# Kernel optimization log

Measured on AMD Instinct MI355X. Metric: run time of the kernel, lower is better.

The kernel has to match this reference:

```python
import jax, jax.numpy as jnp
import numpy as np
from jax import lax

B, N_SITES, FEAT, BOND, OUT = 2048, 128, 64, 32, 256
CORE_SCALE = 0.02  # keeps the 128-step matrix product finite


def setup_inputs() -> dict:
    key = jax.random.key(0)
    ks = jax.random.split(key, 6)
    return {
        "x": jax.random.normal(ks[0], (B, N_SITES, FEAT), dtype=jnp.float32),
        "cores": jax.random.normal(ks[1], (N_SITES, BOND, FEAT, BOND), dtype=jnp.float32) * CORE_SCALE,
        "start": jax.random.normal(ks[2], (1, BOND), dtype=jnp.float32),
        "end": jax.random.normal(ks[3], (BOND, 1), dtype=jnp.float32),
        "fc_w": jax.random.normal(ks[4], (OUT, 1), dtype=jnp.float32),
        "fc_b": jax.random.normal(ks[5], (OUT,), dtype=jnp.float32),
    }


def reference(x, cores, start, end, fc_w, fc_b):
    # x: [B, N, F]; cores: [N, D, F, D]; start: [1, D]; end: [D, 1]
    b = x.shape[0]
    res0 = jnp.broadcast_to(start, (b, start.shape[1]))  # [B, D]

    def step(res, site):
        xi, core = site  # xi: [B, F], core: [D, F, D]
        m = jnp.einsum('bf,dfr->bdr', xi, core)  # per-site transfer matrix [B, D, D]
        return jnp.einsum('bd,bdr->br', res, m), None

    res, _ = lax.scan(step, res0, (jnp.swapaxes(x, 0, 1), cores))
    val = res @ end  # [B, 1]
    return val @ fc_w.T + fc_b  # [B, OUT]
```

## Files before the change

### kernel.cpp

```cpp
#include <hip/hip_runtime.h>


#define NSITES 128
#define FEATD  64
#define BOND   32
#define OUTD   256
#define BT     16
#define SEGLEN 16
#define NSEG   (NSITES / SEGLEN)
#define NBT    (2048 / BT)

#define RSTRIDE 48
#define BSTRIDE 1552

typedef __attribute__((ext_vector_type(4))) float float4v;

__device__ __forceinline__ unsigned pk4_fp8(float a, float b, float c, float d) {
    int v = __builtin_amdgcn_cvt_pk_fp8_f32(a, b, 0, false);
    v = __builtin_amdgcn_cvt_pk_fp8_f32(c, d, v, true);
    return (unsigned)v;
}

__global__ __launch_bounds__(256)
void prep_cores8(const float* __restrict__ cores, unsigned char* __restrict__ core8) {
    __shared__ float tile[FEATD][BOND + 4];
    const int nd = blockIdx.x;
    const int t  = threadIdx.x;
    const float* src = cores + (size_t)nd * (FEATD * BOND);
    {
        int base = t * 8;
        int f = base >> 5, r0 = base & 31;
        float4 v0 = *(const float4*)(src + base);
        float4 v1 = *(const float4*)(src + base + 4);
        tile[f][r0 + 0] = v0.x; tile[f][r0 + 1] = v0.y;
        tile[f][r0 + 2] = v0.z; tile[f][r0 + 3] = v0.w;
        tile[f][r0 + 4] = v1.x; tile[f][r0 + 5] = v1.y;
        tile[f][r0 + 6] = v1.z; tile[f][r0 + 7] = v1.w;
    }
    __syncthreads();
    const int r = t >> 3, f0 = (t & 7) * 8;
    const float s = 16.0f;
    unsigned lo = pk4_fp8(tile[f0 + 0][r] * s, tile[f0 + 1][r] * s,
                          tile[f0 + 2][r] * s, tile[f0 + 3][r] * s);
    unsigned hi = pk4_fp8(tile[f0 + 4][r] * s, tile[f0 + 5][r] * s,
                          tile[f0 + 6][r] * s, tile[f0 + 7][r] * s);
    uint2 w; w.x = lo; w.y = hi;
    *(uint2*)(core8 + ((size_t)nd * BOND + r) * FEATD + f0) = w;
}

__global__ __launch_bounds__(512, 4)
void mps_seg(const float* __restrict__ x, const unsigned char* __restrict__ core8,
             unsigned char* __restrict__ Pout) {
    __shared__ __align__(16) unsigned char MS[BT * BSTRIDE];
    __shared__ __align__(16) unsigned char PS[BT * BSTRIDE];
    __shared__ __align__(16) unsigned char XS[BT * 72];

    const int t    = threadIdx.x;
    const int wave = t >> 6;
    const int lane = t & 63;
    const int cl   = lane & 15;
    const int q    = lane >> 4;
    const int bt   = blockIdx.x;
    const int seg  = blockIdx.y;
    const int b0   = bt * BT;

    {
        int b = t >> 5, d = t & 31;
        unsigned w[8];
#pragma unroll
        for (int dw = 0; dw < 8; ++dw)
            w[dw] = ((d >> 2) == dw) ? (0x58u << ((d & 3) * 8)) : 0u;
        uint4* p = (uint4*)&PS[b * BSTRIDE + d * RSTRIDE];
        p[0] = make_uint4(w[0], w[1], w[2], w[3]);
        p[1] = make_uint4(w[4], w[5], w[6], w[7]);
    }

    const int xb = t >> 5, xf = (t & 31) * 2;
    float2 xf2 = *(const float2*)(x + ((size_t)(b0 + xb) * NSITES + seg * SEGLEN) * FEATD + xf);

    for (int k = 0; k < SEGLEN; ++k) {
        const int n = seg * SEGLEN + k;

        long af[16];
        {
            const unsigned char* base = core8 + (size_t)n * (1024 * FEATD);
#pragma unroll
            for (int i = 0; i < 8; ++i) {
                const unsigned char* p =
                    base + (size_t)((wave * 8 + i) * 16 + cl) * FEATD + q * 8;
                af[i * 2 + 0] = *(const long*)p;
                af[i * 2 + 1] = *(const long*)(p + 32);
            }
        }

        {
            int v = __builtin_amdgcn_cvt_pk_fp8_f32(xf2.x, xf2.y, 0, false);
            *(unsigned short*)&XS[xb * 72 + xf] = (unsigned short)(v & 0xffff);
        }
        __syncthreads();

        long bx0 = *(const long*)&XS[cl * 72 + q * 8];
        long bx1 = *(const long*)&XS[cl * 72 + 32 + q * 8];
        float4v acc[8];
#pragma unroll
        for (int i = 0; i < 8; ++i) {
            float4v z = {0.f, 0.f, 0.f, 0.f};
            z = __builtin_amdgcn_mfma_f32_16x16x32_fp8_fp8(af[i * 2 + 0], bx0, z, 0, 0, 0);
            acc[i] = __builtin_amdgcn_mfma_f32_16x16x32_fp8_fp8(af[i * 2 + 1], bx1, z, 0, 0, 0);
        }

#pragma unroll
        for (int p = 0; p < 2; ++p)
#pragma unroll
            for (int g = 0; g < 4; ++g) {
                unsigned w = pk4_fp8(acc[0 + p][g], acc[2 + p][g],
                                     acc[4 + p][g], acc[6 + p][g]);
                *(unsigned*)&MS[cl * BSTRIDE + (16 * p + 4 * q + g) * RSTRIDE + wave * 4] = w;
            }

        if (k + 1 < SEGLEN)
            xf2 = *(const float2*)(x + ((size_t)(b0 + xb) * NSITES + n + 1) * FEATD + xf);

        __syncthreads();

        long pa[2][2], pb[2][2];
#pragma unroll
        for (int bi = 0; bi < 2; ++bi) {
            int bb = wave * 2 + bi;
#pragma unroll
            for (int h = 0; h < 2; ++h) {
                pa[bi][h] = *(const long*)&MS[bb * BSTRIDE + (h * 16 + cl) * RSTRIDE + q * 8];
                pb[bi][h] = *(const long*)&PS[bb * BSTRIDE + (h * 16 + cl) * RSTRIDE + q * 8];
            }
        }
        float4v pacc[2][2][2];
#pragma unroll
        for (int bi = 0; bi < 2; ++bi)
#pragma unroll
            for (int I = 0; I < 2; ++I)
#pragma unroll
                for (int J = 0; J < 2; ++J) {
                    float4v z = {0.f, 0.f, 0.f, 0.f};
                    pacc[bi][I][J] =
                        __builtin_amdgcn_mfma_f32_16x16x32_fp8_fp8(pa[bi][I], pb[bi][J], z, 0, 0, 0);
                }
#pragma unroll
        for (int bi = 0; bi < 2; ++bi) {
            int bb = wave * 2 + bi;
#pragma unroll
            for (int I = 0; I < 2; ++I)
#pragma unroll
                for (int J = 0; J < 2; ++J) {
                    float4v c = pacc[bi][I][J];
                    unsigned w = pk4_fp8(c[0] * 0.0625f, c[1] * 0.0625f,
                                         c[2] * 0.0625f, c[3] * 0.0625f);
                    *(unsigned*)&PS[bb * BSTRIDE + (J * 16 + cl) * RSTRIDE + I * 16 + q * 4] = w;
                }
        }
    }

    __syncthreads();
    {
        int b = t >> 5, d = t & 31;
        const uint4* p = (const uint4*)&PS[b * BSTRIDE + d * RSTRIDE];
        uint4* g = (uint4*)(Pout + (((size_t)seg * 2048 + b0 + b) * 1024 + d * 32));
        g[0] = p[0];
        g[1] = p[1];
    }
}

__global__ __launch_bounds__(256)
void combine(const unsigned char* __restrict__ Pout, const float* __restrict__ startv,
             const float* __restrict__ endv, const float* __restrict__ fc_w,
             const float* __restrict__ fc_b, float* __restrict__ out) {
    __shared__ __align__(16) unsigned char st[8 * 1024];
    __shared__ float resA[8][33], resB[8][33];
    __shared__ float val[8];
    const int t  = threadIdx.x;
    const int b0 = blockIdx.x * 8;
    const int bb = t >> 5, r = t & 31;

    resA[bb][r] = startv[r];
    for (int s = 0; s < NSEG; ++s) {
        {
            const uint4* g = (const uint4*)(Pout + ((size_t)s * 2048 + b0) * 1024 + (size_t)t * 32);
            uint4* p = (uint4*)&st[t * 32];
            p[0] = g[0];
            p[1] = g[1];
        }
        __syncthreads();
        const float* rin = (s & 1) ? &resB[bb][0] : &resA[bb][0];
        float* rout      = (s & 1) ? &resA[bb][0] : &resB[bb][0];
        float acc = 0.f;
#pragma unroll
        for (int d = 0; d < BOND; ++d) {
            int byte = st[bb * 1024 + d * 32 + r];
            acc += rin[d] * __builtin_amdgcn_cvt_f32_fp8(byte, 0);
        }
        rout[r] = acc * 0.0625f;
        __syncthreads();
    }
    float prod = resA[bb][r] * endv[r];
#pragma unroll
    for (int off = 16; off >= 1; off >>= 1) prod += __shfl_down(prod, off, 32);
    if (r == 0) val[bb] = prod;
    __syncthreads();

    const float v = val[t >> 5];
    const int j0 = (t & 31) * 8;
    const int ob = b0 + (t >> 5);
#pragma unroll
    for (int i = 0; i < 2; ++i) {
        int j = j0 + i * 4;
        float4 w4 = *(const float4*)(fc_w + j);
        float4 bbv = *(const float4*)(fc_b + j);
        float4 o;
        o.x = v * w4.x + bbv.x;
        o.y = v * w4.y + bbv.y;
        o.z = v * w4.z + bbv.z;
        o.w = v * w4.w + bbv.w;
        *(float4*)(out + (size_t)ob * OUTD + j) = o;
    }
}

extern "C" void kernel_launch(void* const* d_in, const int* in_sizes, int n_in,
                              void* d_out, int out_size, void* d_ws, size_t ws_size,
                              hipStream_t stream) {
    const float* x      = (const float*)d_in[0];
    const float* cores  = (const float*)d_in[1];
    const float* startv = (const float*)d_in[2];
    const float* endv   = (const float*)d_in[3];
    const float* fc_w   = (const float*)d_in[4];
    const float* fc_b   = (const float*)d_in[5];
    float* out = (float*)d_out;

    unsigned char* core8 = (unsigned char*)d_ws;
    unsigned char* Pout  = core8 + (size_t)NSITES * 1024 * FEATD;

    prep_cores8<<<NSITES * BOND, 256, 0, stream>>>(cores, core8);
    mps_seg<<<dim3(NBT, NSEG), 512, 0, stream>>>(x, core8, Pout);
    combine<<<2048 / 8, 256, 0, stream>>>(Pout, startv, endv, fc_w, fc_b, out);
}
```

Measured before the change: 244.5 us.

## Process two sites per iteration and keep running product in registers

```diff
diff --git a/kernel.cpp b/kernel.cpp
--- a/kernel.cpp
+++ b/kernel.cpp
@@ -8,10 +8,11 @@
 #define BT     16
 #define SEGLEN 16
 #define NSEG   (NSITES / SEGLEN)
+#define NPAIR  (SEGLEN / 2)
 #define NBT    (2048 / BT)
 
-#define RSTRIDE 48
-#define BSTRIDE 1552
+#define RSTRIDE 36
+#define BSTRIDE 1164
 
 typedef __attribute__((ext_vector_type(4))) float float4v;
 
@@ -19,6 +20,37 @@
     int v = __builtin_amdgcn_cvt_pk_fp8_f32(a, b, 0, false);
     v = __builtin_amdgcn_cvt_pk_fp8_f32(c, d, v, true);
     return (unsigned)v;
+}
+
+__device__ __forceinline__ long ld8(const unsigned char* p) {
+    unsigned lo = *(const unsigned*)p;
+    unsigned hi = *(const unsigned*)(p + 4);
+    return (long)(((unsigned long long)hi << 32) | (unsigned long long)lo);
+}
+
+__device__ __forceinline__ void af_load(long af[16], const unsigned char* __restrict__ core8,
+                                        int n, int wave, int cl, int q) {
+    const unsigned char* base = core8 + (size_t)n * (1024 * FEATD);
+#pragma unroll
+    for (int i = 0; i < 8; ++i) {
+        const unsigned char* p = base + (size_t)((wave * 8 + i) * 16 + cl) * FEATD + q * 8;
+        af[2 * i + 0] = *(const long*)p;
+        af[2 * i + 1] = *(const long*)(p + 32);
+    }
+}
+
+__device__ __forceinline__ long cvt_frag(float4v c0, float4v c1,
+                                         int idxlo, int idxhi, int selhi) {
+    const float s = 0.0625f;
+    int d0 = (int)pk4_fp8(c0[0] * s, c0[1] * s, c0[2] * s, c0[3] * s);
+    int d1 = (int)pk4_fp8(c1[0] * s, c1[1] * s, c1[2] * s, c1[3] * s);
+    int l0 = __builtin_amdgcn_ds_bpermute(idxlo, d0);
+    int l1 = __builtin_amdgcn_ds_bpermute(idxlo, d1);
+    int h0 = __builtin_amdgcn_ds_bpermute(idxhi, d0);
+    int h1 = __builtin_amdgcn_ds_bpermute(idxhi, d1);
+    unsigned lo = (unsigned)(selhi ? l1 : l0);
+    unsigned hi = (unsigned)(selhi ? h1 : h0);
+    return (long)(((unsigned long long)hi << 32) | (unsigned long long)lo);
 }
 
 __global__ __launch_bounds__(256)
@@ -51,9 +83,10 @@
 __global__ __launch_bounds__(512, 4)
 void mps_seg(const float* __restrict__ x, const unsigned char* __restrict__ core8,
              unsigned char* __restrict__ Pout) {
-    __shared__ __align__(16) unsigned char MS[BT * BSTRIDE];
-    __shared__ __align__(16) unsigned char PS[BT * BSTRIDE];
-    __shared__ __align__(16) unsigned char XS[BT * 72];
+    __shared__ __align__(16) unsigned char MA[BT * BSTRIDE];
+    __shared__ __align__(16) unsigned char MB[BT * BSTRIDE];
+    __shared__ __align__(16) unsigned char NT[BT * BSTRIDE];
+    __shared__ __align__(16) unsigned char XS[2][2][BT * 72];
 
     const int t    = threadIdx.x;
     const int wave = t >> 6;
@@ -63,109 +96,152 @@
     const int bt   = blockIdx.x;
     const int seg  = blockIdx.y;
     const int b0   = bt * BT;
-
+    const int xb   = t >> 5, xf = (t & 31) * 2;
+
+    const int idxlo = (cl + 16 * ((2 * q) & 3)) << 2;
+    const int idxhi = (cl + 16 * ((2 * q + 1) & 3)) << 2;
+    const int selhi = q >> 1;
+
+    long ps[2][2];
+#pragma unroll
+    for (int J = 0; J < 2; ++J) {
+        int row = J * 16 + cl;
+        int jj  = row - 8 * q;
+        long v  = (jj >= 0 && jj < 8) ? (long)(0x58ULL << (8 * jj)) : 0L;
+        ps[0][J] = v;
+        ps[1][J] = v;
+    }
+
+    const int n0 = seg * SEGLEN;
+
+    const float* xptr = x + ((size_t)(b0 + xb) * NSITES + n0) * FEATD + xf;
+    float2 xa  = *(const float2*)xptr;
+    float2 xbv = *(const float2*)(xptr + FEATD);
     {
-        int b = t >> 5, d = t & 31;
-        unsigned w[8];
-#pragma unroll
-        for (int dw = 0; dw < 8; ++dw)
-            w[dw] = ((d >> 2) == dw) ? (0x58u << ((d & 3) * 8)) : 0u;
-        uint4* p = (uint4*)&PS[b * BSTRIDE + d * RSTRIDE];
-        p[0] = make_uint4(w[0], w[1], w[2], w[3]);
-        p[1] = make_uint4(w[4], w[5], w[6], w[7]);
-    }
-
-    const int xb = t >> 5, xf = (t & 31) * 2;
-    float2 xf2 = *(const float2*)(x + ((size_t)(b0 + xb) * NSITES + seg * SEGLEN) * FEATD + xf);
-
-    for (int k = 0; k < SEGLEN; ++k) {
-        const int n = seg * SEGLEN + k;
-
-        long af[16];
+        int v0 = __builtin_amdgcn_cvt_pk_fp8_f32(xa.x, xa.y, 0, false);
+        *(unsigned short*)&XS[0][0][xb * 72 + xf] = (unsigned short)(v0 & 0xffff);
+        int v1 = __builtin_amdgcn_cvt_pk_fp8_f32(xbv.x, xbv.y, 0, false);
+        *(unsigned short*)&XS[0][1][xb * 72 + xf] = (unsigned short)(v1 & 0xffff);
+    }
+    long afa[16];
+    af_load(afa, core8, n0, wave, cl, q);
+    __syncthreads();
+
+    for (int j = 0; j < NPAIR; ++j) {
+        const int n = n0 + 2 * j;
+
         {
-            const unsigned char* base = core8 + (size_t)n * (1024 * FEATD);
+            const unsigned char* xsA = &XS[j & 1][0][0];
+            const unsigned char* xsB = &XS[j & 1][1][0];
+            long bxa0 = *(const long*)(xsA + cl * 72 + q * 8);
+            long bxa1 = *(const long*)(xsA + cl * 72 + 32 + q * 8);
+            long bxb0 = *(const long*)(xsB + cl * 72 + q * 8);
+            long bxb1 = *(const long*)(xsB + cl * 72 + 32 + q * 8);
+
+            long afb[16];
+            af_load(afb, core8, n + 1, wave, cl, q);
+
+            float4v acc[8];
 #pragma unroll
             for (int i = 0; i < 8; ++i) {
-                const unsigned char* p =
-                    base + (size_t)((wave * 8 + i) * 16 + cl) * FEATD + q * 8;
-                af[i * 2 + 0] = *(const long*)p;
-                af[i * 2 + 1] = *(const long*)(p + 32);
-            }
-        }
-
-        {
-            int v = __builtin_amdgcn_cvt_pk_fp8_f32(xf2.x, xf2.y, 0, false);
-            *(unsigned short*)&XS[xb * 72 + xf] = (unsigned short)(v & 0xffff);
+                float4v z = {0.f, 0.f, 0.f, 0.f};
+                z = __builtin_amdgcn_mfma_f32_16x16x32_fp8_fp8(afa[2 * i + 0], bxa0, z, 0, 0, 0);
+                acc[i] = __builtin_amdgcn_mfma_f32_16x16x32_fp8_fp8(afa[2 * i + 1], bxa1, z, 0, 0, 0);
+            }
+#pragma unroll
+            for (int i = 0; i < 8; ++i) {
+                unsigned w = pk4_fp8(acc[i][0], acc[i][1], acc[i][2], acc[i][3]);
+                *(unsigned*)&MA[cl * BSTRIDE + (wave * 4 + (i >> 1)) * RSTRIDE
+                                + (i & 1) * 16 + q * 4] = w;
+            }
+
+            if (j + 1 < NPAIR) {
+                const float* xp = x + ((size_t)(b0 + xb) * NSITES + n + 2) * FEATD + xf;
+                xa  = *(const float2*)xp;
+                xbv = *(const float2*)(xp + FEATD);
+            }
+
+            float4v accb[8];
+#pragma unroll
+            for (int i = 0; i < 8; ++i) {
+                float4v z = {0.f, 0.f, 0.f, 0.f};
+                z = __builtin_amdgcn_mfma_f32_16x16x32_fp8_fp8(afb[2 * i + 0], bxb0, z, 0, 0, 0);
+                accb[i] = __builtin_amdgcn_mfma_f32_16x16x32_fp8_fp8(afb[2 * i + 1], bxb1, z, 0, 0, 0);
+            }
+#pragma unroll
+            for (int p = 0; p < 2; ++p)
+#pragma unroll
+                for (int g = 0; g < 4; ++g) {
+                    unsigned w = pk4_fp8(accb[0 + p][g], accb[2 + p][g],
+                                         accb[4 + p][g], accb[6 + p][g]);
+                    *(unsigned*)&MB[cl * BSTRIDE + (16 * p + 4 * q + g) * RSTRIDE
+                                    + wave * 4] = w;
+                }
         }
         __syncthreads();
 
-        long bx0 = *(const long*)&XS[cl * 72 + q * 8];
-        long bx1 = *(const long*)&XS[cl * 72 + 32 + q * 8];
-        float4v acc[8];
-#pragma unroll
-        for (int i = 0; i < 8; ++i) {
-            float4v z = {0.f, 0.f, 0.f, 0.f};
-            z = __builtin_amdgcn_mfma_f32_16x16x32_fp8_fp8(af[i * 2 + 0], bx0, z, 0, 0, 0);
-            acc[i] = __builtin_amdgcn_mfma_f32_16x16x32_fp8_fp8(af[i * 2 + 1], bx1, z, 0, 0, 0);
+        {
+            if (j + 1 < NPAIR) {
+                int v0 = __builtin_amdgcn_cvt_pk_fp8_f32(xa.x, xa.y, 0, false);
+                *(unsigned short*)&XS[(j + 1) & 1][0][xb * 72 + xf] = (unsigned short)(v0 & 0xffff);
+                int v1 = __builtin_amdgcn_cvt_pk_fp8_f32(xbv.x, xbv.y, 0, false);
+                *(unsigned short*)&XS[(j + 1) & 1][1][xb * 72 + xf] = (unsigned short)(v1 & 0xffff);
+                af_load(afa, core8, n + 2, wave, cl, q);
+            }
+
+#pragma unroll
+            for (int bi = 0; bi < 2; ++bi) {
+                const int bb = wave * 2 + bi;
+                const unsigned char* mab = &MA[bb * BSTRIDE];
+                const unsigned char* mbb = &MB[bb * BSTRIDE];
+                long pa0 = ld8(mab + cl * RSTRIDE + q * 8);
+                long pa1 = ld8(mab + (16 + cl) * RSTRIDE + q * 8);
+                long pb0 = ld8(mbb + cl * RSTRIDE + q * 8);
+                long pb1 = ld8(mbb + (16 + cl) * RSTRIDE + q * 8);
+                float4v z00 = {0.f, 0.f, 0.f, 0.f}, z01 = {0.f, 0.f, 0.f, 0.f};
+                float4v z10 = {0.f, 0.f, 0.f, 0.f}, z11 = {0.f, 0.f, 0.f, 0.f};
+                z00 = __builtin_amdgcn_mfma_f32_16x16x32_fp8_fp8(pa0, pb0, z00, 0, 0, 0);
+                z01 = __builtin_amdgcn_mfma_f32_16x16x32_fp8_fp8(pa0, pb1, z01, 0, 0, 0);
+                z10 = __builtin_amdgcn_mfma_f32_16x16x32_fp8_fp8(pa1, pb0, z10, 0, 0, 0);
+                z11 = __builtin_amdgcn_mfma_f32_16x16x32_fp8_fp8(pa1, pb1, z11, 0, 0, 0);
+                unsigned char* nb = &NT[bb * BSTRIDE];
+                const float s = 0.0625f;
+                unsigned w00 = pk4_fp8(z00[0] * s, z00[1] * s, z00[2] * s, z00[3] * s);
+                unsigned w01 = pk4_fp8(z01[0] * s, z01[1] * s, z01[2] * s, z01[3] * s);
+                unsigned w10 = pk4_fp8(z10[0] * s, z10[1] * s, z10[2] * s, z10[3] * s);
+                unsigned w11 = pk4_fp8(z11[0] * s, z11[1] * s, z11[2] * s, z11[3] * s);
+                *(unsigned*)&nb[(0 * 16 + cl) * RSTRIDE + 0 * 16 + q * 4] = w00;
+                *(unsigned*)&nb[(1 * 16 + cl) * RSTRIDE + 0 * 16 + q * 4] = w01;
+                *(unsigned*)&nb[(0 * 16 + cl) * RSTRIDE + 1 * 16 + q * 4] = w10;
+                *(unsigned*)&nb[(1 * 16 + cl) * RSTRIDE + 1 * 16 + q * 4] = w11;
+            }
+
+#pragma unroll
+            for (int bi = 0; bi < 2; ++bi) {
+                const int bb = wave * 2 + bi;
+                const unsigned char* nb = &NT[bb * BSTRIDE];
+                long ca0 = ld8(nb + cl * RSTRIDE + q * 8);
+                long ca1 = ld8(nb + (16 + cl) * RSTRIDE + q * 8);
+                float4v c00 = {0.f, 0.f, 0.f, 0.f}, c01 = {0.f, 0.f, 0.f, 0.f};
+                float4v c10 = {0.f, 0.f, 0.f, 0.f}, c11 = {0.f, 0.f, 0.f, 0.f};
+                c00 = __builtin_amdgcn_mfma_f32_16x16x32_fp8_fp8(ca0, ps[bi][0], c00, 0, 0, 0);
+                c01 = __builtin_amdgcn_mfma_f32_16x16x32_fp8_fp8(ca0, ps[bi][1], c01, 0, 0, 0);
+                c10 = __builtin_amdgcn_mfma_f32_16x16x32_fp8_fp8(ca1, ps[bi][0], c10, 0, 0, 0);
+                c11 = __builtin_amdgcn_mfma_f32_16x16x32_fp8_fp8(ca1, ps[bi][1], c11, 0, 0, 0);
+                ps[bi][0] = cvt_frag(c00, c10, idxlo, idxhi, selhi);
+                ps[bi][1] = cvt_frag(c01, c11, idxlo, idxhi, selhi);
+            }
         }
-
-#pragma unroll
-        for (int p = 0; p < 2; ++p)
-#pragma unroll
-            for (int g = 0; g < 4; ++g) {
-                unsigned w = pk4_fp8(acc[0 + p][g], acc[2 + p][g],
-                                     acc[4 + p][g], acc[6 + p][g]);
-                *(unsigned*)&MS[cl * BSTRIDE + (16 * p + 4 * q + g) * RSTRIDE + wave * 4] = w;
-            }
-
-        if (k + 1 < SEGLEN)
-            xf2 = *(const float2*)(x + ((size_t)(b0 + xb) * NSITES + n + 1) * FEATD + xf);
-
         __syncthreads();
-
-        long pa[2][2], pb[2][2];
-#pragma unroll
-        for (int bi = 0; bi < 2; ++bi) {
-            int bb = wave * 2 + bi;
-#pragma unroll
-            for (int h = 0; h < 2; ++h) {
-                pa[bi][h] = *(const long*)&MS[bb * BSTRIDE + (h * 16 + cl) * RSTRIDE + q * 8];
-                pb[bi][h] = *(const long*)&PS[bb * BSTRIDE + (h * 16 + cl) * RSTRIDE + q * 8];
-            }
-        }
-        float4v pacc[2][2][2];
-#pragma unroll
-        for (int bi = 0; bi < 2; ++bi)
-#pragma unroll
-            for (int I = 0; I < 2; ++I)
-#pragma unroll
-                for (int J = 0; J < 2; ++J) {
-                    float4v z = {0.f, 0.f, 0.f, 0.f};
-                    pacc[bi][I][J] =
-                        __builtin_amdgcn_mfma_f32_16x16x32_fp8_fp8(pa[bi][I], pb[bi][J], z, 0, 0, 0);
-                }
-#pragma unroll
-        for (int bi = 0; bi < 2; ++bi) {
-            int bb = wave * 2 + bi;
-#pragma unroll
-            for (int I = 0; I < 2; ++I)
-#pragma unroll
-                for (int J = 0; J < 2; ++J) {
-                    float4v c = pacc[bi][I][J];
-                    unsigned w = pk4_fp8(c[0] * 0.0625f, c[1] * 0.0625f,
-                                         c[2] * 0.0625f, c[3] * 0.0625f);
-                    *(unsigned*)&PS[bb * BSTRIDE + (J * 16 + cl) * RSTRIDE + I * 16 + q * 4] = w;
-                }
-        }
-    }
-
-    __syncthreads();
-    {
-        int b = t >> 5, d = t & 31;
-        const uint4* p = (const uint4*)&PS[b * BSTRIDE + d * RSTRIDE];
-        uint4* g = (uint4*)(Pout + (((size_t)seg * 2048 + b0 + b) * 1024 + d * 32));
-        g[0] = p[0];
-        g[1] = p[1];
+    }
+
+#pragma unroll
+    for (int bi = 0; bi < 2; ++bi) {
+        const int bb = wave * 2 + bi;
+        unsigned char* gp = Pout + ((size_t)seg * 2048 + b0 + bb) * 1024;
+#pragma unroll
+        for (int J = 0; J < 2; ++J)
+            *(long*)(gp + (J * 16 + cl) * 32 + q * 8) = ps[bi][J];
     }
 }
 
```

Result: no change. 245.0 us (+0.2%).
